# Kernel tuning notes

Measured on AMD Instinct MI355X. Metric: run time of the kernel, lower is better.

Reference implementation:

```python
import jax, jax.numpy as jnp
import numpy as np

N, E, D, L = 50000, 800000, 128, 2
EPS = 1e-10


def mobius_add(x, y, c):
    # c: shape [1], broadcasts against [N,1]
    xy = jnp.sum(x * y, axis=-1, keepdims=True)
    x2 = jnp.sum(x * x, axis=-1, keepdims=True)
    y2 = jnp.sum(y * y, axis=-1, keepdims=True)
    num = (1 + 2 * c * xy + c * y2) * x + (1 - c * x2) * y
    den = 1 + 2 * c * xy + (c ** 2) * x2 * y2
    return num / den


def log_map(x, y, c):
    ym = mobius_add(-x, y, c)
    n = jnp.maximum(jnp.linalg.norm(ym, axis=-1, keepdims=True), EPS)
    sc = jnp.sqrt(c)
    return (2.0 / sc) * jnp.arctanh(sc * n) * ym / n


def exp_map(x, v, c):
    n = jnp.maximum(jnp.linalg.norm(v, axis=-1, keepdims=True), EPS)
    sc = jnp.sqrt(c)
    second = jnp.tanh(sc * n / 2.0) * v / (sc * n)
    return mobius_add(x, second, c)


def l2norm(x):
    return x / jnp.maximum(jnp.linalg.norm(x, axis=-1, keepdims=True), 1e-12)


def mean_agg(h, src, dst, n_nodes):
    # copy_u + mean reduce: mean of h[src] grouped by dst; zero-degree -> 0
    msum = jax.ops.segment_sum(h[src], dst, num_segments=n_nodes)
    deg = jax.ops.segment_sum(jnp.ones((src.shape[0], 1), h.dtype), dst, num_segments=n_nodes)
    return msum / jnp.maximum(deg, 1.0)


def setup_inputs() -> dict:
    key = jax.random.key(0)
    ks = jax.random.split(key, 12)
    scale = 1.0 / np.sqrt(D)
    return {
        "src": jax.random.randint(ks[0], (E,), 0, N, dtype=jnp.int32),
        "dst": jax.random.randint(ks[1], (E,), 0, N, dtype=jnp.int32),
        "e_emb": jax.random.normal(ks[2], (N, D), dtype=jnp.float32),
        "b_emb": 0.01 * jax.random.normal(ks[3], (N, D), dtype=jnp.float32),  # inside Poincare ball
        "s_emb": jax.random.normal(ks[4], (N, D), dtype=jnp.float32),
        "e_W": scale * jax.random.normal(ks[5], (L, D, D), dtype=jnp.float32),
        "e_b": jnp.zeros((L, D), dtype=jnp.float32),
        "b_W": scale * jax.random.normal(ks[6], (L, D, D), dtype=jnp.float32),
        "b_b": jnp.zeros((L, D), dtype=jnp.float32),
        "s_W": scale * jax.random.normal(ks[7], (L, D, D), dtype=jnp.float32),
        "s_b": jnp.zeros((L, D), dtype=jnp.float32),
        "b_curvature": jnp.ones((1,), dtype=jnp.float32),
        "s_curvature": jnp.ones((1,), dtype=jnp.float32),
    }


def reference(src, dst, e_emb, b_emb, s_emb, e_W, e_b, b_W, b_b, s_W, s_b, b_curvature, s_curvature):
    n = e_emb.shape[0]
    origin = jnp.zeros((1, b_emb.shape[-1]), dtype=b_emb.dtype)
    for l in range(L):
        # Euclidean: transform -> mean aggregate -> LeakyReLU(0.2)
        h = e_emb @ e_W[l].T + e_b[l]
        e_emb = mean_agg(h, src, dst, n)
        e_emb = jnp.where(e_emb > 0, e_emb, 0.2 * e_emb)
        # Hyperbolic: log map to tangent -> transform -> mean aggregate -> exp map
        tangent = log_map(origin, b_emb, b_curvature)
        hb = tangent @ b_W[l].T + b_b[l]
        neigh_b = mean_agg(hb, src, dst, n)
        b_emb = exp_map(origin, neigh_b, b_curvature)
        # Spherical: normalize -> transform -> normalize -> mean aggregate -> normalize
        hs = l2norm(l2norm(s_emb) @ s_W[l].T + s_b[l])
        s_emb = l2norm(mean_agg(hs, src, dst, n))
    return (e_emb, b_emb, s_emb)
```

## Files before the change

kernel.cpp:

```cpp
#include <hip/hip_runtime.h>
#include <math.h>

#define DD 128
typedef unsigned int   u32;
typedef unsigned short u16;
typedef short bf16x8 __attribute__((ext_vector_type(8)));
typedef float f32x4  __attribute__((ext_vector_type(4)));

__device__ __forceinline__ float lo2f(u32 p){ return __uint_as_float(p << 16); }
__device__ __forceinline__ float hi2f(u32 p){ return __uint_as_float(p & 0xFFFF0000u); }
__device__ __forceinline__ u16 f2bf(float f){
    u32 u = __float_as_uint(f);
    return (u16)((u + 0x7fffu + ((u >> 16) & 1u)) >> 16);
}

__global__ void k_hist(const int* __restrict__ dst, int* __restrict__ deg, int E){
    int i = blockIdx.x*256 + threadIdx.x;
    if (i < E) atomicAdd(&deg[dst[i]], 1);
}

__global__ void k_chunksum(const int* __restrict__ deg, int* __restrict__ csum,
                           float* __restrict__ invdeg, int n){
    __shared__ int sdata[256];
    int t = threadIdx.x;
    int i0 = blockIdx.x*512 + t*2;
    int a = (i0     < n) ? deg[i0]   : 0;
    int b = (i0 + 1 < n) ? deg[i0+1] : 0;
    if (i0     < n) invdeg[i0]   = 1.0f / (float)max(a, 1);
    if (i0 + 1 < n) invdeg[i0+1] = 1.0f / (float)max(b, 1);
    sdata[t] = a + b; __syncthreads();
    for (int off = 128; off > 0; off >>= 1){
        if (t < off) sdata[t] += sdata[t+off];
        __syncthreads();
    }
    if (t == 0) csum[blockIdx.x] = sdata[0];
}

__global__ void k_scanchunks(int* __restrict__ csum, int nchunks,
                             int* __restrict__ row_ptr, int n){
    __shared__ int s[256];
    __shared__ int carry_sh;
    int t = threadIdx.x;
    if (t == 0) carry_sh = 0;
    __syncthreads();
    for (int base = 0; base < nchunks; base += 256){
        int i = base + t;
        int v = (i < nchunks) ? csum[i] : 0;
        s[t] = v;
        __syncthreads();
        for (int off = 1; off < 256; off <<= 1){
            int u = (t >= off) ? s[t-off] : 0;
            __syncthreads();
            s[t] += u;
            __syncthreads();
        }
        int carry = carry_sh;
        int excl  = carry + s[t] - v;
        if (i < nchunks) csum[i] = excl;
        int tot = s[255];
        __syncthreads();
        if (t == 0) carry_sh = carry + tot;
        __syncthreads();
    }
    if (t == 0) row_ptr[n] = carry_sh;
}

__global__ void k_scanwithin(const int* __restrict__ deg, const int* __restrict__ csum,
                             int* __restrict__ row_ptr, int* __restrict__ cursor, int n){
    __shared__ int s[256];
    int t = threadIdx.x;
    int i0 = blockIdx.x*512 + t*2;
    int a = (i0     < n) ? deg[i0]   : 0;
    int b = (i0 + 1 < n) ? deg[i0+1] : 0;
    int tsum = a + b;
    s[t] = tsum; __syncthreads();
    for (int off = 1; off < 256; off <<= 1){
        int v = (t >= off) ? s[t-off] : 0;
        __syncthreads();
        s[t] += v;
        __syncthreads();
    }
    int excl = s[t] - tsum + csum[blockIdx.x];
    if (i0     < n){ row_ptr[i0]   = excl;     cursor[i0]   = excl;     }
    if (i0 + 1 < n){ row_ptr[i0+1] = excl + a; cursor[i0+1] = excl + a; }
}

__global__ void k_fill(const int* __restrict__ src, const int* __restrict__ dst,
                       int* __restrict__ cursor, int* __restrict__ sorted_src, int E){
    int i = blockIdx.x*256 + threadIdx.x;
    if (i < E){
        int p = atomicAdd(&cursor[dst[i]], 1);
        sorted_src[p] = src[i];
    }
}

__global__ void k_w2b3(const float* __restrict__ w0, const float* __restrict__ w1,
                       const float* __restrict__ w2,
                       u16* __restrict__ o0, u16* __restrict__ o1, u16* __restrict__ o2,
                       int nw){
    int i = blockIdx.x*256 + threadIdx.x;
    if (i >= nw) return;
    const float* s = (blockIdx.y == 0) ? w0 : (blockIdx.y == 1) ? w1 : w2;
    u16*         o = (blockIdx.y == 0) ? o0 : (blockIdx.y == 1) ? o1 : o2;
    o[i] = f2bf(s[i]);
}

template<int PRE, int POST>
__device__ __forceinline__ void gemm_body(const float* __restrict__ X, const u16* __restrict__ Wb,
                                          const float* __restrict__ bias, u16* __restrict__ Y,
                                          int n_rows, const float* __restrict__ cptr){
    int t = threadIdx.x;
    int wave = t >> 6, lane = t & 63;
    int q = lane >> 4, m = lane & 15;
    int rowbase = blockIdx.x*64 + wave*16;
    int gr = min(rowbase + m, n_rows - 1);

    float4 xv[8];
    const float4* xp = (const float4*)(X + (size_t)gr*DD);
    #pragma unroll
    for (int c = 0; c < 4; c++){
        xv[2*c]   = xp[c*8 + q*2];
        xv[2*c+1] = xp[c*8 + q*2 + 1];
    }

    float scale = 1.0f;
    if (PRE != 0){
        float ss = 0.f;
        #pragma unroll
        for (int i = 0; i < 8; i++)
            ss += xv[i].x*xv[i].x + xv[i].y*xv[i].y + xv[i].z*xv[i].z + xv[i].w*xv[i].w;
        ss += __shfl_xor(ss, 16, 64);
        ss += __shfl_xor(ss, 32, 64);
        float nrm = sqrtf(ss);
        if (PRE == 1){
            float c  = cptr[0];
            c = (c > 0.f && c < 1e30f) ? c : 1.0f;
            float sc = sqrtf(c);
            float n2 = fmaxf(nrm, 1e-10f);
            float a  = fminf(sc*n2, 0.99999994f);
            scale = (2.0f/sc) * atanhf(a) / n2;
        } else {
            scale = 1.0f / fmaxf(nrm, 1e-12f);
        }
    }

    bf16x8 af[4];
    #pragma unroll
    for (int c = 0; c < 4; c++){
        const float* xf = (const float*)&xv[2*c];
        #pragma unroll
        for (int j = 0; j < 8; j++) af[c][j] = (short)f2bf(xf[j]*scale);
    }

    f32x4 acc[8];
    #pragma unroll
    for (int tl = 0; tl < 8; tl++) acc[tl] = (f32x4){0.f,0.f,0.f,0.f};

    const u16* wb = Wb + (size_t)m*DD + q*8;
    #pragma unroll
    for (int c = 0; c < 4; c++){
        #pragma unroll
        for (int tl = 0; tl < 8; tl++){
            bf16x8 bfr = *(const bf16x8*)(wb + (size_t)tl*16*DD + c*32);
            acc[tl] = __builtin_amdgcn_mfma_f32_16x16x32_bf16(af[c], bfr, acc[tl], 0, 0, 0);
        }
    }

    #pragma unroll
    for (int tl = 0; tl < 8; tl++){
        float bv = bias[tl*16 + m];
        #pragma unroll
        for (int r = 0; r < 4; r++) acc[tl][r] += bv;
    }
    if (POST == 1){
        float ssr[4] = {0.f,0.f,0.f,0.f};
        #pragma unroll
        for (int tl = 0; tl < 8; tl++)
            #pragma unroll
            for (int r = 0; r < 4; r++) ssr[r] += acc[tl][r]*acc[tl][r];
        #pragma unroll
        for (int r = 0; r < 4; r++){
            float s = ssr[r];
            s += __shfl_xor(s, 1, 64);
            s += __shfl_xor(s, 2, 64);
            s += __shfl_xor(s, 4, 64);
            s += __shfl_xor(s, 8, 64);
            float sc = 1.0f / fmaxf(sqrtf(s), 1e-12f);
            #pragma unroll
            for (int tl = 0; tl < 8; tl++) acc[tl][r] *= sc;
        }
    }
    #pragma unroll
    for (int r = 0; r < 4; r++){
        int grow = rowbase + q*4 + r;
        if (grow < n_rows){
            #pragma unroll
            for (int tl = 0; tl < 8; tl++)
                Y[(size_t)grow*DD + tl*16 + m] = f2bf(acc[tl][r]);
        }
    }
}

__global__ __launch_bounds__(256, 4)
void k_gemm3(const float* __restrict__ Xe, const float* __restrict__ Xb, const float* __restrict__ Xs,
             const u16* __restrict__ We, const u16* __restrict__ Wh, const u16* __restrict__ Ws,
             const float* __restrict__ be, const float* __restrict__ bb, const float* __restrict__ bs,
             u16* __restrict__ Ye, u16* __restrict__ Yb, u16* __restrict__ Ys,
             int n_rows, const float* __restrict__ cptr){
    if (blockIdx.y == 0)      gemm_body<0,0>(Xe, We, be, Ye, n_rows, cptr);
    else if (blockIdx.y == 1) gemm_body<1,0>(Xb, Wh, bb, Yb, n_rows, cptr);
    else                      gemm_body<2,1>(Xs, Ws, bs, Ys, n_rows, cptr);
}

__device__ __forceinline__ void acc8(float* a, uint4 p){
    a[0] += lo2f(p.x); a[1] += hi2f(p.x);
    a[2] += lo2f(p.y); a[3] += hi2f(p.y);
    a[4] += lo2f(p.z); a[5] += hi2f(p.z);
    a[6] += lo2f(p.w); a[7] += hi2f(p.w);
}

__global__ __launch_bounds__(256)
void k_agg3(const u32* __restrict__ he, const u32* __restrict__ hb, const u32* __restrict__ hs,
            const int* __restrict__ row_ptr, const int* __restrict__ sorted_src,
            const float* __restrict__ invdeg,
            float* __restrict__ out_e, float* __restrict__ out_b, float* __restrict__ out_s,
            int n_rows, const float* __restrict__ cptr){
    int wid = (blockIdx.x*256 + threadIdx.x) >> 6;
    if (wid >= n_rows) return;
    int lane = threadIdx.x & 63;
    int g = lane >> 4, c = lane & 15;
    int beg = row_ptr[wid], end = row_ptr[wid+1];
    int coff = c*4;

    float ae[8], ab[8], as_[8];
    #pragma unroll
    for (int i = 0; i < 8; i++){ ae[i] = 0.f; ab[i] = 0.f; as_[i] = 0.f; }

    int p = beg + g;
    for (; p + 4 < end; p += 8){
        size_t o0 = (size_t)sorted_src[p]  *64 + coff;
        size_t o1 = (size_t)sorted_src[p+4]*64 + coff;
        uint4 e0 = *(const uint4*)(he + o0);
        uint4 b0 = *(const uint4*)(hb + o0);
        uint4 s0 = *(const uint4*)(hs + o0);
        uint4 e1 = *(const uint4*)(he + o1);
        uint4 b1 = *(const uint4*)(hb + o1);
        uint4 s1 = *(const uint4*)(hs + o1);
        acc8(ae, e0); acc8(ab, b0); acc8(as_, s0);
        acc8(ae, e1); acc8(ab, b1); acc8(as_, s1);
    }
    if (p < end){
        size_t o0 = (size_t)sorted_src[p]*64 + coff;
        uint4 e0 = *(const uint4*)(he + o0);
        uint4 b0 = *(const uint4*)(hb + o0);
        uint4 s0 = *(const uint4*)(hs + o0);
        acc8(ae, e0); acc8(ab, b0); acc8(as_, s0);
    }

    #pragma unroll
    for (int i = 0; i < 8; i++){
        ae[i]  += __shfl_xor(ae[i],  16, 64); ae[i]  += __shfl_xor(ae[i],  32, 64);
        ab[i]  += __shfl_xor(ab[i],  16, 64); ab[i]  += __shfl_xor(ab[i],  32, 64);
        as_[i] += __shfl_xor(as_[i], 16, 64); as_[i] += __shfl_xor(as_[i], 32, 64);
    }
    float inv = invdeg[wid];
    #pragma unroll
    for (int i = 0; i < 8; i++){ ae[i] *= inv; ab[i] *= inv; as_[i] *= inv; }

    float ssb = 0.f, sss = 0.f;
    #pragma unroll
    for (int i = 0; i < 8; i++){ ssb += ab[i]*ab[i]; sss += as_[i]*as_[i]; }
    #pragma unroll
    for (int msk = 1; msk < 16; msk <<= 1){
        ssb += __shfl_xor(ssb, msk, 64);
        sss += __shfl_xor(sss, msk, 64);
    }

    if (g == 0){
        float o[8];
        #pragma unroll
        for (int i = 0; i < 8; i++) o[i] = ae[i] > 0.f ? ae[i] : 0.2f*ae[i];
        float4* dstp = (float4*)(out_e + (size_t)wid*DD + c*8);
        dstp[0] = make_float4(o[0],o[1],o[2],o[3]);
        dstp[1] = make_float4(o[4],o[5],o[6],o[7]);
    } else if (g == 1){
        float cc = cptr[0];
        cc = (cc > 0.f && cc < 1e30f) ? cc : 1.0f;
        float sc = sqrtf(cc);
        float n2 = fmaxf(sqrtf(ssb), 1e-10f);
        float scale = tanhf(sc*n2*0.5f) / (sc*n2);
        float4* dstp = (float4*)(out_b + (size_t)wid*DD + c*8);
        dstp[0] = make_float4(ab[0]*scale, ab[1]*scale, ab[2]*scale, ab[3]*scale);
        dstp[1] = make_float4(ab[4]*scale, ab[5]*scale, ab[6]*scale, ab[7]*scale);
    } else if (g == 2){
        float scale = 1.0f / fmaxf(sqrtf(sss), 1e-12f);
        float4* dstp = (float4*)(out_s + (size_t)wid*DD + c*8);
        dstp[0] = make_float4(as_[0]*scale, as_[1]*scale, as_[2]*scale, as_[3]*scale);
        dstp[1] = make_float4(as_[4]*scale, as_[5]*scale, as_[6]*scale, as_[7]*scale);
    }
}

extern "C" void kernel_launch(void* const* d_in, const int* in_sizes, int n_in,
                              void* d_out, int out_size, void* d_ws, size_t ws_size,
                              hipStream_t stream){
    const int*   src = (const int*)d_in[0];
    const int*   dst = (const int*)d_in[1];
    const float* emb_in[3] = {(const float*)d_in[2], (const float*)d_in[3], (const float*)d_in[4]};
    const float* W_in[3]   = {(const float*)d_in[5], (const float*)d_in[7], (const float*)d_in[9]};
    const float* b_in[3]   = {(const float*)d_in[6], (const float*)d_in[8], (const float*)d_in[10]};
    const float* b_c       = (const float*)d_in[11];

    const int E  = in_sizes[0];
    const int ND = in_sizes[2];
    const int N  = ND / DD;
    const int Lnum = in_sizes[5] / (DD*DD);
    const int nw = Lnum*DD*DD;
    const int nchunks = (N + 511) / 512;

    char* w = (char*)d_ws;
    auto alloc = [&](size_t bytes)->char*{
        char* p = w; w += (bytes + 255) & ~(size_t)255; return p;
    };
    u32*   hE        = (u32*)  alloc((size_t)ND*2);
    u32*   hB        = (u32*)  alloc((size_t)ND*2);
    u32*   hS        = (u32*)  alloc((size_t)ND*2);
    u16*   Wb[3];
    for (int i = 0; i < 3; i++) Wb[i] = (u16*)alloc((size_t)nw*2);
    float* invdeg    = (float*)alloc((size_t)N*4);
    int*   deg       = (int*)  alloc((size_t)N*4);
    int*   row_ptr   = (int*)  alloc((size_t)(N+1)*4);
    int*   cursor    = (int*)  alloc((size_t)N*4);
    int*   csum      = (int*)  alloc((size_t)nchunks*4);
    int*   sorted_src= (int*)  alloc((size_t)E*4);
    (void)ws_size; (void)n_in; (void)out_size;

    float* out_e = (float*)d_out;
    float* out_b = out_e + ND;
    float* out_s = out_e + 2*ND;

    hipMemsetAsync(deg, 0, (size_t)N*4, stream);

    const int TB = 256;
    k_w2b3<<<dim3((nw+TB-1)/TB, 3), TB, 0, stream>>>(W_in[0], W_in[1], W_in[2],
                                                     Wb[0], Wb[1], Wb[2], nw);
    k_hist<<<(E+TB-1)/TB, TB, 0, stream>>>(dst, deg, E);
    k_chunksum<<<nchunks, 256, 0, stream>>>(deg, csum, invdeg, N);
    k_scanchunks<<<1, 256, 0, stream>>>(csum, nchunks, row_ptr, N);
    k_scanwithin<<<nchunks, 256, 0, stream>>>(deg, csum, row_ptr, cursor, N);
    k_fill<<<(E+TB-1)/TB, TB, 0, stream>>>(src, dst, cursor, sorted_src, E);

    const int rowblocks  = (N + 3) / 4;
    const int gemmblocks = (N + 63) / 64;

    const float* se = emb_in[0];
    const float* sb = emb_in[1];
    const float* ss = emb_in[2];

    for (int l = 0; l < Lnum; l++){
        k_gemm3<<<dim3(gemmblocks, 3), 256, 0, stream>>>(
            se, sb, ss,
            Wb[0] + (size_t)l*DD*DD, Wb[1] + (size_t)l*DD*DD, Wb[2] + (size_t)l*DD*DD,
            b_in[0] + (size_t)l*DD,  b_in[1] + (size_t)l*DD,  b_in[2] + (size_t)l*DD,
            (u16*)hE, (u16*)hB, (u16*)hS, N, b_c);
        k_agg3<<<rowblocks, 256, 0, stream>>>(hE, hB, hS, row_ptr, sorted_src, invdeg,
                                              out_e, out_b, out_s, N, b_c);
        se = out_e; sb = out_b; ss = out_s;
    }
}
```

Baseline: 512.5 us.

## Partition aggregation by XCD over column slices and cancel log/exp between layers

The fused three-way gather is replaced by an aggregation kernel that uses the block index modulo 8 to give each XCD a fixed column slice of an interleaved Euclidean/hyperbolic bf16 table, or of the spherical table. Each XCD's L2 then only has to hold a fraction of the gathered feature data instead of every full row. Between layers the exp map and the following log map cancel, so intermediate layers store the raw mean and the next GEMM skips its log-map prologue. Intermediate spherical outputs are also left unnormalised, since the next GEMM normalises its input anyway. The last layer adds a separate finalisation pass that applies the exp map and normalisation, at the cost of extra fp32 traffic and slight numerical differences from skipping the tanh/arctanh round trip.

```diff
diff --git a/kernel.cpp b/kernel.cpp
--- a/kernel.cpp
+++ b/kernel.cpp
@@ -108,7 +108,7 @@
 template<int PRE, int POST>
 __device__ __forceinline__ void gemm_body(const float* __restrict__ X, const u16* __restrict__ Wb,
                                           const float* __restrict__ bias, u16* __restrict__ Y,
-                                          int n_rows, const float* __restrict__ cptr){
+                                          int RS, int n_rows, const float* __restrict__ cptr){
     int t = threadIdx.x;
     int wave = t >> 6, lane = t & 63;
     int q = lane >> 4, m = lane & 15;
@@ -196,20 +196,21 @@
         if (grow < n_rows){
             #pragma unroll
             for (int tl = 0; tl < 8; tl++)
-                Y[(size_t)grow*DD + tl*16 + m] = f2bf(acc[tl][r]);
-        }
-    }
-}
-
+                Y[(size_t)grow*RS + tl*16 + m] = f2bf(acc[tl][r]);
+        }
+    }
+}
+
+template<int PREB>
 __global__ __launch_bounds__(256, 4)
 void k_gemm3(const float* __restrict__ Xe, const float* __restrict__ Xb, const float* __restrict__ Xs,
              const u16* __restrict__ We, const u16* __restrict__ Wh, const u16* __restrict__ Ws,
              const float* __restrict__ be, const float* __restrict__ bb, const float* __restrict__ bs,
-             u16* __restrict__ Ye, u16* __restrict__ Yb, u16* __restrict__ Ys,
+             u16* __restrict__ hEB, u16* __restrict__ hS,
              int n_rows, const float* __restrict__ cptr){
-    if (blockIdx.y == 0)      gemm_body<0,0>(Xe, We, be, Ye, n_rows, cptr);
-    else if (blockIdx.y == 1) gemm_body<1,0>(Xb, Wh, bb, Yb, n_rows, cptr);
-    else                      gemm_body<2,1>(Xs, Ws, bs, Ys, n_rows, cptr);
+    if (blockIdx.y == 0)      gemm_body<0,0>(Xe, We, be, hEB,       256, n_rows, cptr);
+    else if (blockIdx.y == 1) gemm_body<PREB,0>(Xb, Wh, bb, hEB+128, 256, n_rows, cptr);
+    else                      gemm_body<2,1>(Xs, Ws, bs, hS,        128, n_rows, cptr);
 }
 
 __device__ __forceinline__ void acc8(float* a, uint4 p){
@@ -220,84 +221,112 @@
 }
 
 __global__ __launch_bounds__(256)
-void k_agg3(const u32* __restrict__ he, const u32* __restrict__ hb, const u32* __restrict__ hs,
+void k_aggT(const u32* __restrict__ hEB, const u32* __restrict__ hS,
             const int* __restrict__ row_ptr, const int* __restrict__ sorted_src,
             const float* __restrict__ invdeg,
-            float* __restrict__ out_e, float* __restrict__ out_b, float* __restrict__ out_s,
-            int n_rows, const float* __restrict__ cptr){
+            float* __restrict__ oE, float* __restrict__ oB, float* __restrict__ oS,
+            int n_rows){
+    int xcd = blockIdx.x & 7;
+    int idx = blockIdx.x >> 3;
+
+    const u32* table; int rs, coff, nodebase, hi, outcol0, path;
+    {
+        int hf  = xcd & 1;
+        int loA = (int)(((long long)n_rows * hf) >> 1);
+        int hiA = (int)(((long long)n_rows * (hf+1)) >> 1);
+        int nbA = (hiA - loA + 15) >> 4;
+        if (idx < nbA){
+            int cA = xcd >> 1;
+            table = hEB; rs = 128; coff = cA*32;
+            nodebase = loA + idx*16; hi = hiA;
+            path = cA >> 1; outcol0 = (cA & 1)*64;
+        } else {
+            int i2 = idx - nbA;
+            int qd = xcd & 3;
+            int loB = (int)(((long long)n_rows * qd) >> 2);
+            int hiB = (int)(((long long)n_rows * (qd+1)) >> 2);
+            int nbB = (hiB - loB + 15) >> 4;
+            if (i2 >= nbB) return;
+            int cS = xcd >> 2;
+            table = hS; rs = 64; coff = cS*32;
+            nodebase = loB + i2*16; hi = hiB;
+            path = 2; outcol0 = cS*64;
+        }
+    }
+    float* dest = (path == 0) ? oE : (path == 1) ? oB : oS;
+    bool leaky = (path == 0);
+
+    int w = threadIdx.x >> 6, lane = threadIdx.x & 63;
+    int g = lane >> 3, l8 = lane & 7;
+    const u32* tbl = table + coff + l8*4;
+
+    for (int k = 0; k < 4; k++){
+        int v = nodebase + w*4 + k;
+        if (v >= hi) break;
+        int beg = row_ptr[v], end = row_ptr[v+1];
+        float a[8];
+        #pragma unroll
+        for (int i = 0; i < 8; i++) a[i] = 0.f;
+
+        int p = beg + g;
+        for (; p + 8 < end; p += 16){
+            int i0 = sorted_src[p];
+            int i1 = sorted_src[p+8];
+            uint4 c0 = *(const uint4*)(tbl + (size_t)i0*rs);
+            uint4 c1 = *(const uint4*)(tbl + (size_t)i1*rs);
+            acc8(a, c0); acc8(a, c1);
+        }
+        if (p < end){
+            int i0 = sorted_src[p];
+            uint4 c0 = *(const uint4*)(tbl + (size_t)i0*rs);
+            acc8(a, c0);
+        }
+
+        #pragma unroll
+        for (int i = 0; i < 8; i++){
+            a[i] += __shfl_xor(a[i], 8, 64);
+            a[i] += __shfl_xor(a[i], 16, 64);
+            a[i] += __shfl_xor(a[i], 32, 64);
+        }
+        if (g == 0){
+            float inv = invdeg[v];
+            float o[8];
+            #pragma unroll
+            for (int i = 0; i < 8; i++){
+                float x = a[i]*inv;
+                o[i] = leaky ? (x > 0.f ? x : 0.2f*x) : x;
+            }
+            float4* dp = (float4*)(dest + (size_t)v*DD + outcol0 + l8*8);
+            dp[0] = make_float4(o[0],o[1],o[2],o[3]);
+            dp[1] = make_float4(o[4],o[5],o[6],o[7]);
+        }
+    }
+}
+
+__global__ __launch_bounds__(256)
+void k_final(const float* __restrict__ tb, const float* __restrict__ ts,
+             float* __restrict__ ob, float* __restrict__ os,
+             int n_rows, const float* __restrict__ cptr){
     int wid = (blockIdx.x*256 + threadIdx.x) >> 6;
     if (wid >= n_rows) return;
     int lane = threadIdx.x & 63;
-    int g = lane >> 4, c = lane & 15;
-    int beg = row_ptr[wid], end = row_ptr[wid+1];
-    int coff = c*4;
-
-    float ae[8], ab[8], as_[8];
-    #pragma unroll
-    for (int i = 0; i < 8; i++){ ae[i] = 0.f; ab[i] = 0.f; as_[i] = 0.f; }
-
-    int p = beg + g;
-    for (; p + 4 < end; p += 8){
-        size_t o0 = (size_t)sorted_src[p]  *64 + coff;
-        size_t o1 = (size_t)sorted_src[p+4]*64 + coff;
-        uint4 e0 = *(const uint4*)(he + o0);
-        uint4 b0 = *(const uint4*)(hb + o0);
-        uint4 s0 = *(const uint4*)(hs + o0);
-        uint4 e1 = *(const uint4*)(he + o1);
-        uint4 b1 = *(const uint4*)(hb + o1);
-        uint4 s1 = *(const uint4*)(hs + o1);
-        acc8(ae, e0); acc8(ab, b0); acc8(as_, s0);
-        acc8(ae, e1); acc8(ab, b1); acc8(as_, s1);
-    }
-    if (p < end){
-        size_t o0 = (size_t)sorted_src[p]*64 + coff;
-        uint4 e0 = *(const uint4*)(he + o0);
-        uint4 b0 = *(const uint4*)(hb + o0);
-        uint4 s0 = *(const uint4*)(hs + o0);
-        acc8(ae, e0); acc8(ab, b0); acc8(as_, s0);
-    }
-
-    #pragma unroll
-    for (int i = 0; i < 8; i++){
-        ae[i]  += __shfl_xor(ae[i],  16, 64); ae[i]  += __shfl_xor(ae[i],  32, 64);
-        ab[i]  += __shfl_xor(ab[i],  16, 64); ab[i]  += __shfl_xor(ab[i],  32, 64);
-        as_[i] += __shfl_xor(as_[i], 16, 64); as_[i] += __shfl_xor(as_[i], 32, 64);
-    }
-    float inv = invdeg[wid];
-    #pragma unroll
-    for (int i = 0; i < 8; i++){ ae[i] *= inv; ab[i] *= inv; as_[i] *= inv; }
-
-    float ssb = 0.f, sss = 0.f;
-    #pragma unroll
-    for (int i = 0; i < 8; i++){ ssb += ab[i]*ab[i]; sss += as_[i]*as_[i]; }
-    #pragma unroll
-    for (int msk = 1; msk < 16; msk <<= 1){
-        ssb += __shfl_xor(ssb, msk, 64);
-        sss += __shfl_xor(sss, msk, 64);
-    }
-
-    if (g == 0){
-        float o[8];
-        #pragma unroll
-        for (int i = 0; i < 8; i++) o[i] = ae[i] > 0.f ? ae[i] : 0.2f*ae[i];
-        float4* dstp = (float4*)(out_e + (size_t)wid*DD + c*8);
-        dstp[0] = make_float4(o[0],o[1],o[2],o[3]);
-        dstp[1] = make_float4(o[4],o[5],o[6],o[7]);
-    } else if (g == 1){
-        float cc = cptr[0];
-        cc = (cc > 0.f && cc < 1e30f) ? cc : 1.0f;
-        float sc = sqrtf(cc);
-        float n2 = fmaxf(sqrtf(ssb), 1e-10f);
-        float scale = tanhf(sc*n2*0.5f) / (sc*n2);
-        float4* dstp = (float4*)(out_b + (size_t)wid*DD + c*8);
-        dstp[0] = make_float4(ab[0]*scale, ab[1]*scale, ab[2]*scale, ab[3]*scale);
-        dstp[1] = make_float4(ab[4]*scale, ab[5]*scale, ab[6]*scale, ab[7]*scale);
-    } else if (g == 2){
-        float scale = 1.0f / fmaxf(sqrtf(sss), 1e-12f);
-        float4* dstp = (float4*)(out_s + (size_t)wid*DD + c*8);
-        dstp[0] = make_float4(as_[0]*scale, as_[1]*scale, as_[2]*scale, as_[3]*scale);
-        dstp[1] = make_float4(as_[4]*scale, as_[5]*scale, as_[6]*scale, as_[7]*scale);
-    }
+    float2 vb = *(const float2*)(tb + (size_t)wid*DD + lane*2);
+    float2 vs = *(const float2*)(ts + (size_t)wid*DD + lane*2);
+    float ssb = vb.x*vb.x + vb.y*vb.y;
+    float sss = vs.x*vs.x + vs.y*vs.y;
+    #pragma unroll
+    for (int m = 32; m > 0; m >>= 1){
+        ssb += __shfl_xor(ssb, m, 64);
+        sss += __shfl_xor(sss, m, 64);
+    }
+    float cc = cptr[0];
+    cc = (cc > 0.f && cc < 1e30f) ? cc : 1.0f;
+    float sc = sqrtf(cc);
+    float nb = fmaxf(sqrtf(ssb), 1e-10f);
+    float scb = tanhf(sc*nb*0.5f) / (sc*nb);
+    float scs = 1.0f / fmaxf(sqrtf(sss), 1e-12f);
+    *(float2*)(ob + (size_t)wid*DD + lane*2) = make_float2(vb.x*scb, vb.y*scb);
+    *(float2*)(os + (size_t)wid*DD + lane*2) = make_float2(vs.x*scs, vs.y*scs);
 }
 
 extern "C" void kernel_launch(void* const* d_in, const int* in_sizes, int n_in,
@@ -321,9 +350,10 @@
     auto alloc = [&](size_t bytes)->char*{
         char* p = w; w += (bytes + 255) & ~(size_t)255; return p;
     };
-    u32*   hE        = (u32*)  alloc((size_t)ND*2);
-    u32*   hB        = (u32*)  alloc((size_t)ND*2);
+    u32*   hEB       = (u32*)  alloc((size_t)ND*4);
     u32*   hS        = (u32*)  alloc((size_t)ND*2);
+    float* tb        = (float*)alloc((size_t)ND*4);
+    float* ts        = (float*)alloc((size_t)ND*4);
     u16*   Wb[3];
     for (int i = 0; i < 3; i++) Wb[i] = (u16*)alloc((size_t)nw*2);
     float* invdeg    = (float*)alloc((size_t)N*4);
@@ -349,21 +379,38 @@
     k_scanwithin<<<nchunks, 256, 0, stream>>>(deg, csum, row_ptr, cursor, N);
     k_fill<<<(E+TB-1)/TB, TB, 0, stream>>>(src, dst, cursor, sorted_src, E);
 
-    const int rowblocks  = (N + 3) / 4;
     const int gemmblocks = (N + 63) / 64;
+    const int nbA = (((N+1)/2) + 15) / 16;
+    const int nbB = (((N+3)/4) + 15) / 16;
+    const int aggblocks = 8 * (nbA + nbB);
+    const int finblocks = (N + 3) / 4;
 
     const float* se = emb_in[0];
     const float* sb = emb_in[1];
     const float* ss = emb_in[2];
 
     for (int l = 0; l < Lnum; l++){
-        k_gemm3<<<dim3(gemmblocks, 3), 256, 0, stream>>>(
-            se, sb, ss,
-            Wb[0] + (size_t)l*DD*DD, Wb[1] + (size_t)l*DD*DD, Wb[2] + (size_t)l*DD*DD,
-            b_in[0] + (size_t)l*DD,  b_in[1] + (size_t)l*DD,  b_in[2] + (size_t)l*DD,
-            (u16*)hE, (u16*)hB, (u16*)hS, N, b_c);
-        k_agg3<<<rowblocks, 256, 0, stream>>>(hE, hB, hS, row_ptr, sorted_src, invdeg,
-                                              out_e, out_b, out_s, N, b_c);
+        bool last = (l == Lnum - 1);
+        if (l == 0)
+            k_gemm3<1><<<dim3(gemmblocks, 3), 256, 0, stream>>>(
+                se, sb, ss,
+                Wb[0] + (size_t)l*DD*DD, Wb[1] + (size_t)l*DD*DD, Wb[2] + (size_t)l*DD*DD,
+                b_in[0] + (size_t)l*DD,  b_in[1] + (size_t)l*DD,  b_in[2] + (size_t)l*DD,
+                (u16*)hEB, (u16*)hS, N, b_c);
+        else
+            k_gemm3<0><<<dim3(gemmblocks, 3), 256, 0, stream>>>(
+                se, sb, ss,
+                Wb[0] + (size_t)l*DD*DD, Wb[1] + (size_t)l*DD*DD, Wb[2] + (size_t)l*DD*DD,
+                b_in[0] + (size_t)l*DD,  b_in[1] + (size_t)l*DD,  b_in[2] + (size_t)l*DD,
+                (u16*)hEB, (u16*)hS, N, b_c);
+
+        float* dB = last ? tb : out_b;
+        float* dS = last ? ts : out_s;
+        k_aggT<<<aggblocks, 256, 0, stream>>>(hEB, hS, row_ptr, sorted_src, invdeg,
+                                              out_e, dB, dS, N);
+        if (last)
+            k_final<<<finblocks, 256, 0, stream>>>(tb, ts, out_b, out_s, N, b_c);
+
         se = out_e; sb = out_b; ss = out_s;
     }
 }
```

Result: slower. 567.7 us (+10.8%).
